# Optimization experiments

Hardware: AMD Instinct MI355X
Metric: run time of the kernel (lower is better)

Reference implementation:

```python
import jax, jax.numpy as jnp
import numpy as np

N_NODES = 50000
N_EDGES = 600000
IN_DIM = 128
H_DIM = 128
OUT_DIM = 128
N_REL = 8
N_BASES = 8
N_GRAPHS = 256


def _lin(key, i, o):
    return jax.random.normal(key, (i, o), dtype=jnp.float32) / np.sqrt(i)


def setup_inputs() -> dict:
    key = jax.random.key(0)
    ks = jax.random.split(key, 16)
    inp = {}
    inp["features"] = jax.random.normal(ks[0], (N_NODES, IN_DIM), dtype=jnp.float32)
    inp["src"] = jax.random.randint(ks[1], (N_EDGES,), 0, N_NODES, dtype=jnp.int32)
    inp["dst"] = jax.random.randint(ks[2], (N_EDGES,), 0, N_NODES, dtype=jnp.int32)
    inp["etype"] = jax.random.randint(ks[3], (N_EDGES,), 0, N_REL, dtype=jnp.int32)
    inp["node2graph"] = jnp.sort(jax.random.randint(ks[4], (N_NODES,), 0, N_GRAPHS, dtype=jnp.int32))
    # RelGraphConv basis-decomposed weights: bases [B,in,out], comp [R,B], bias [out]
    inp["bases1"] = jax.random.normal(ks[5], (N_BASES, IN_DIM, H_DIM), dtype=jnp.float32) / np.sqrt(IN_DIM)
    inp["comp1"] = jax.random.normal(ks[6], (N_REL, N_BASES), dtype=jnp.float32) / np.sqrt(N_BASES)
    inp["bias1"] = jnp.zeros((H_DIM,), dtype=jnp.float32)
    inp["bases2"] = jax.random.normal(ks[7], (N_BASES, H_DIM, H_DIM), dtype=jnp.float32) / np.sqrt(H_DIM)
    inp["comp2"] = jax.random.normal(ks[8], (N_REL, N_BASES), dtype=jnp.float32) / np.sqrt(N_BASES)
    inp["bias2"] = jnp.zeros((H_DIM,), dtype=jnp.float32)
    inp["bases3"] = jax.random.normal(ks[9], (N_BASES, H_DIM, OUT_DIM), dtype=jnp.float32) / np.sqrt(H_DIM)
    inp["comp3"] = jax.random.normal(ks[10], (N_REL, N_BASES), dtype=jnp.float32) / np.sqrt(N_BASES)
    inp["bias3"] = jnp.zeros((OUT_DIM,), dtype=jnp.float32)
    # attention gate + MLP head
    inp["gate_w"] = _lin(ks[11], OUT_DIM, 1)
    inp["gate_b"] = jnp.zeros((1,), dtype=jnp.float32)
    inp["fc1_w"] = _lin(ks[12], OUT_DIM, 100)
    inp["fc1_b"] = jnp.zeros((100,), dtype=jnp.float32)
    inp["fc2_w"] = _lin(ks[13], 100, 64)
    inp["fc2_b"] = jnp.zeros((64,), dtype=jnp.float32)
    inp["fc3_w"] = _lin(ks[14], 64, 1)
    inp["fc3_b"] = jnp.zeros((1,), dtype=jnp.float32)
    return inp


def _rgcn_layer(x, bases, comp, bias, src, dst, etype):
    # basis decomposition: W_r = sum_b comp[r,b] * bases[b]
    W = jnp.einsum('rb,bio->rio', comp, bases)            # [R, in, out]
    h_all = jnp.einsum('ni,rio->nro', x, W)               # [N, R, out]
    msg = h_all[src, etype]                               # gather per-edge: W_{etype} x_src, [E, out]
    agg = jax.ops.segment_sum(msg, dst, num_segments=x.shape[0])
    return agg + bias


def _segment_softmax(gate, seg, num_segments):
    # gate: [N, 1]; softmax per graph segment
    m = jax.ops.segment_max(gate, seg, num_segments=num_segments)
    e = jnp.exp(gate - m[seg])
    s = jax.ops.segment_sum(e, seg, num_segments=num_segments)
    return e / s[seg]


def reference(features, bases1, comp1, bias1, bases2, comp2, bias2,
              bases3, comp3, bias3, gate_w, gate_b,
              fc1_w, fc1_b, fc2_w, fc2_b, fc3_w, fc3_b,
              src, dst, etype, node2graph):
    h = _rgcn_layer(features, bases1, comp1, bias1, src, dst, etype)
    h = jax.nn.relu(h)  # dropout=0.0 -> identity
    h = _rgcn_layer(h, bases2, comp2, bias2, src, dst, etype)
    h = jax.nn.relu(h)
    h = _rgcn_layer(h, bases3, comp3, bias3, src, dst, etype)
    # GlobalAttentionPooling
    gate = h @ gate_w + gate_b                            # [N, 1]
    gate = _segment_softmax(gate, node2graph, N_GRAPHS)
    readout = jax.ops.segment_sum(h * gate, node2graph, num_segments=N_GRAPHS)  # [G, out]
    # MLP classifier + sigmoid
    z = jax.nn.relu(readout @ fc1_w + fc1_b)
    z = jax.nn.relu(z @ fc2_w + fc2_b)
    z = z @ fc3_w + fc3_b
    return jax.nn.sigmoid(z).squeeze(-1)                  # [G]
```

## Files before the change

### kernel.cpp

```cpp
#include <hip/hip_runtime.h>
#include <hip/hip_bf16.h>
#include <math.h>

#define N_NODES 50000
#define N_EDGES 600000
#define DIM 128
#define N_REL 8
#define N_GRAPHS 256
#define NBN 32
#define NBLK ((N_NODES + NBN - 1) / NBN)
#define KDIM (N_REL * DIM)
#define NKEY (N_NODES * N_REL)
#define SEG 1024
#define NSEG2 391

typedef __attribute__((ext_vector_type(8))) short short8;
typedef __attribute__((ext_vector_type(4))) float floatx4;
typedef __attribute__((ext_vector_type(4))) float f32x4;
typedef unsigned int uint;
typedef unsigned short ushort;

static __device__ __forceinline__ int lower_bound_i(const int* a, int n, int v) {
    int lo = 0, hi = n;
    while (lo < hi) { int mid = (lo + hi) >> 1; if (a[mid] < v) lo = mid + 1; else hi = mid; }
    return lo;
}

static __device__ __forceinline__ uint2 split2(float x, float y) {
    uint ux = __float_as_uint(x);
    uint hx = (ux + 0x7FFFu + ((ux >> 16) & 1u)) & 0xFFFF0000u;
    float rx = x - __uint_as_float(hx);
    uint urx = __float_as_uint(rx);
    uint lx = (urx + 0x7FFFu + ((urx >> 16) & 1u)) >> 16;
    uint uy = __float_as_uint(y);
    uint hy = (uy + 0x7FFFu + ((uy >> 16) & 1u)) & 0xFFFF0000u;
    float ry = y - __uint_as_float(hy);
    uint ury = __float_as_uint(ry);
    uint ly = (ury + 0x7FFFu + ((ury >> 16) & 1u)) >> 16;
    return make_uint2((hx >> 16) | (hy & 0xFFFF0000u), lx | (ly << 16));
}

__global__ void k_count(const int* __restrict__ dst, const int* __restrict__ etype,
                        int* __restrict__ counts, int e) {
    int i = blockIdx.x * blockDim.x + threadIdx.x;
    if (i < e) atomicAdd(&counts[dst[i] * 8 + etype[i]], 1);
}

__global__ __launch_bounds__(256) void k_scan_seg(const int* __restrict__ counts,
                                                  int* __restrict__ segscan,
                                                  int* __restrict__ segtot) {
    const int b = blockIdx.x, t = threadIdx.x;
    const int base = b * SEG + t * 4;
    const int4 v = *(const int4*)(counts + base);
    const int s0 = v.x, s1 = s0 + v.y, s2 = s1 + v.z, s3 = s2 + v.w;
    __shared__ int sl[256];
    sl[t] = s3;
    __syncthreads();
    for (int off = 1; off < 256; off <<= 1) {
        int add = (t >= off) ? sl[t - off] : 0;
        __syncthreads();
        sl[t] += add;
        __syncthreads();
    }
    const int tp = sl[t] - s3;
    int4 o;
    o.x = tp; o.y = tp + s0; o.z = tp + s1; o.w = tp + s2;
    *(int4*)(segscan + base) = o;
    if (t == 255) segtot[b] = sl[255];
}

__global__ __launch_bounds__(512) void k_scan_tot(const int* __restrict__ segtot,
                                                  int* __restrict__ segbase) {
    const int t = threadIdx.x;
    const int v = (t < NSEG2) ? segtot[t] : 0;
    __shared__ int sl[512];
    sl[t] = v;
    __syncthreads();
    for (int off = 1; off < 512; off <<= 1) {
        int u = (t >= off) ? sl[t - off] : 0;
        __syncthreads();
        sl[t] += u;
        __syncthreads();
    }
    if (t < NSEG2) segbase[t] = sl[t] - v;
    if (t == NSEG2) segbase[NSEG2] = sl[NSEG2 - 1];
}

__global__ void k_scan_fin(const int* __restrict__ segscan, const int* __restrict__ segbase,
                           int* __restrict__ offsets, int* __restrict__ cursor) {
    const int i = blockIdx.x * blockDim.x + threadIdx.x;
    if (i < NKEY) {
        const int val = segbase[i >> 10] + segscan[i];
        offsets[i] = val;
        cursor[i] = val;
    } else if (i == NKEY) {
        offsets[NKEY] = segbase[NSEG2];
    }
}

__global__ void k_fill(const int* __restrict__ src, const int* __restrict__ dst,
                       const int* __restrict__ etype, int* cursor,
                       int* __restrict__ edges, int e) {
    int i = blockIdx.x * blockDim.x + threadIdx.x;
    if (i < e) {
        const int et = etype[i];
        int pos = atomicAdd(&cursor[dst[i] * 8 + et], 1);
        edges[pos] = src[i] | (et << 16);
    }
}

__global__ void k_packW(const float* __restrict__ bases, const float* __restrict__ comp,
                        ushort* __restrict__ Whi, ushort* __restrict__ Wlo) {
    int id = blockIdx.x * blockDim.x + threadIdx.x;
    int nn = id & 127, k = id >> 7;
    int r = k >> 7, dk = k & 127;
    const float* cp = comp + r * 8;
    float v = 0.f;
#pragma unroll
    for (int b = 0; b < 8; b++) v = fmaf(cp[b], bases[((size_t)b * 128 + dk) * 128 + nn], v);
    uint u = __float_as_uint(v);
    uint hu = (u + 0x7FFFu + ((u >> 16) & 1u)) & 0xFFFF0000u;
    float rf = v - __uint_as_float(hu);
    uint ur = __float_as_uint(rf);
    uint lu = (ur + 0x7FFFu + ((ur >> 16) & 1u)) >> 16;
    int kt = k >> 5, kk = k & 31;
    int off = kt * 4096 + nn * 32 + kk;
    Whi[off] = (ushort)(hu >> 16);
    Wlo[off] = (ushort)lu;
}

template <bool RELU, bool GATE>
__global__ __launch_bounds__(512, 4) void k_layer(
    const float* __restrict__ xin, float* __restrict__ hout,
    const int* __restrict__ edges, const int* __restrict__ offsets,
    const ushort* __restrict__ Whi, const ushort* __restrict__ Wlo,
    const float* __restrict__ bias,
    const float* __restrict__ gw, const float* __restrict__ gb,
    float* __restrict__ gate) {
    __shared__ ushort sHi[16 * 1024];
    __shared__ ushort sLo[16 * 1024];
    __shared__ float sgatep[NBN][8];
    const int tid = threadIdx.x;
    const int lane = tid & 63;
    const int w = tid >> 6;
    const int q2 = lane >> 4, mm = lane & 15;
    const int xev = (mm ^ q2) * 8;
    const int xod = ((mm ^ q2) ^ 4) * 8;
    const int aq = q2 * 256;
    const int n0 = w * 16 + mm;
    const ushort* bph = Whi + n0 * 32 + q2 * 8;
    const ushort* bpl = Wlo + n0 * 32 + q2 * 8;
    floatx4 acc0 = {0.f, 0.f, 0.f, 0.f};
    floatx4 acc1 = {0.f, 0.f, 0.f, 0.f};

    const int hw = tid >> 5, l5 = tid & 31;
    const int d0 = l5 * 4;
    const int kt_off = l5 >> 3;
    const int q = (l5 >> 1) & 3;
    const int jb = (l5 & 1) * 4;

#pragma unroll
    for (int h = 0; h < 2; ++h) {
        {
            uint4 z = make_uint4(0u, 0u, 0u, 0u);
#pragma unroll
            for (int i = 0; i < 4; ++i) {
                ((uint4*)sHi)[tid + i * 512] = z;
                ((uint4*)sLo)[tid + i * 512] = z;
            }
        }
        __syncthreads();

        for (int v = 0; v < 2; ++v) {
            const int m = hw * 2 + v;
            const int n = blockIdx.x * NBN + m;
            int e0 = 0, e1 = 0;
            if (n < N_NODES) { e0 = offsets[n * 8 + h * 4]; e1 = offsets[n * 8 + h * 4 + 4]; }
            f32x4 tmp = (f32x4)0.f;
            int rcur = -1;

#define FLUSH_FRAG(RRR)                                                        \
            {                                                                  \
                const int ktp = (RRR) * 4 + kt_off;                            \
                const int chunk = q * 32 + ((m ^ q) ^ ((ktp & 1) << 2));       \
                const int uoff = ktp * 1024 + chunk * 8 + jb;                  \
                const uint2 p01 = split2(tmp.x, tmp.y);                        \
                const uint2 p23 = split2(tmp.z, tmp.w);                        \
                *(uint2*)(sHi + uoff) = make_uint2(p01.x, p23.x);              \
                *(uint2*)(sLo + uoff) = make_uint2(p01.y, p23.y);              \
            }

#define CONSUME_EDGE(PK, VV)                                                   \
            {                                                                  \
                const int r_ = ((PK) >> 16) & 3;                               \
                if (r_ != rcur) {                                              \
                    if (rcur >= 0) FLUSH_FRAG(rcur);                           \
                    rcur = r_;                                                 \
                    tmp = (VV);                                                \
                } else {                                                       \
                    tmp += (VV);                                               \
                }                                                              \
            }

            const int nb4 = (e1 - e0) >> 2;
            int pa0 = 0, pa1 = 0, pa2 = 0, pa3 = 0;
            int pb0 = 0, pb1 = 0, pb2 = 0, pb3 = 0;
            f32x4 va0, va1, va2, va3;
            if (0 < nb4) { const int ee = e0;     pa0 = edges[ee]; pa1 = edges[ee + 1]; pa2 = edges[ee + 2]; pa3 = edges[ee + 3]; }
            if (1 < nb4) { const int ee = e0 + 4; pb0 = edges[ee]; pb1 = edges[ee + 1]; pb2 = edges[ee + 2]; pb3 = edges[ee + 3]; }
            if (0 < nb4) {
                va0 = *(const f32x4*)(xin + (size_t)(pa0 & 0xFFFF) * DIM + d0);
                va1 = *(const f32x4*)(xin + (size_t)(pa1 & 0xFFFF) * DIM + d0);
                va2 = *(const f32x4*)(xin + (size_t)(pa2 & 0xFFFF) * DIM + d0);
                va3 = *(const f32x4*)(xin + (size_t)(pa3 & 0xFFFF) * DIM + d0);
            }
            for (int i = 0; i < nb4; ++i) {
                int pc0 = 0, pc1 = 0, pc2 = 0, pc3 = 0;
                if (i + 2 < nb4) {
                    const int ee = e0 + (i + 2) * 4;
                    pc0 = edges[ee]; pc1 = edges[ee + 1]; pc2 = edges[ee + 2]; pc3 = edges[ee + 3];
                }
                f32x4 vb0, vb1, vb2, vb3;
                if (i + 1 < nb4) {
                    vb0 = *(const f32x4*)(xin + (size_t)(pb0 & 0xFFFF) * DIM + d0);
                    vb1 = *(const f32x4*)(xin + (size_t)(pb1 & 0xFFFF) * DIM + d0);
                    vb2 = *(const f32x4*)(xin + (size_t)(pb2 & 0xFFFF) * DIM + d0);
                    vb3 = *(const f32x4*)(xin + (size_t)(pb3 & 0xFFFF) * DIM + d0);
                }
                CONSUME_EDGE(pa0, va0);
                CONSUME_EDGE(pa1, va1);
                CONSUME_EDGE(pa2, va2);
                CONSUME_EDGE(pa3, va3);
                pa0 = pb0; pa1 = pb1; pa2 = pb2; pa3 = pb3;
                pb0 = pc0; pb1 = pc1; pb2 = pc2; pb3 = pc3;
                va0 = vb0; va1 = vb1; va2 = vb2; va3 = vb3;
            }
            {
                const int et = e0 + nb4 * 4;
                const int rem = e1 - et;
                int pt0 = 0, pt1 = 0, pt2 = 0;
                if (rem > 0) pt0 = edges[et];
                if (rem > 1) pt1 = edges[et + 1];
                if (rem > 2) pt2 = edges[et + 2];
                f32x4 vt0, vt1, vt2;
                if (rem > 0) vt0 = *(const f32x4*)(xin + (size_t)(pt0 & 0xFFFF) * DIM + d0);
                if (rem > 1) vt1 = *(const f32x4*)(xin + (size_t)(pt1 & 0xFFFF) * DIM + d0);
                if (rem > 2) vt2 = *(const f32x4*)(xin + (size_t)(pt2 & 0xFFFF) * DIM + d0);
                if (rem > 0) CONSUME_EDGE(pt0, vt0);
                if (rem > 1) CONSUME_EDGE(pt1, vt1);
                if (rem > 2) CONSUME_EDGE(pt2, vt2);
            }
            if (rcur >= 0) FLUSH_FRAG(rcur);
#undef CONSUME_EDGE
#undef FLUSH_FRAG
        }
        __syncthreads();

        for (int kt = 0; kt < 16; kt += 2) {
            {
                const int ktg = h * 16 + kt;
                const ushort* ap = sHi + kt * 1024 + aq;
                const ushort* alp = sLo + kt * 1024 + aq;
                const short8 ah0 = *(const short8*)(ap + xev);
                const short8 ah1 = *(const short8*)(ap + 128 + xev);
                const short8 al0 = *(const short8*)(alp + xev);
                const short8 al1 = *(const short8*)(alp + 128 + xev);
                const short8 bh = *(const short8*)(bph + ktg * 4096);
                const short8 bl = *(const short8*)(bpl + ktg * 4096);
                acc0 = __builtin_amdgcn_mfma_f32_16x16x32_bf16(ah0, bh, acc0, 0, 0, 0);
                acc1 = __builtin_amdgcn_mfma_f32_16x16x32_bf16(ah1, bh, acc1, 0, 0, 0);
                acc0 = __builtin_amdgcn_mfma_f32_16x16x32_bf16(ah0, bl, acc0, 0, 0, 0);
                acc1 = __builtin_amdgcn_mfma_f32_16x16x32_bf16(ah1, bl, acc1, 0, 0, 0);
                acc0 = __builtin_amdgcn_mfma_f32_16x16x32_bf16(al0, bh, acc0, 0, 0, 0);
                acc1 = __builtin_amdgcn_mfma_f32_16x16x32_bf16(al1, bh, acc1, 0, 0, 0);
            }
            {
                const int kto = kt + 1;
                const int ktg = h * 16 + kto;
                const ushort* ap = sHi + kto * 1024 + aq;
                const ushort* alp = sLo + kto * 1024 + aq;
                const short8 ah0 = *(const short8*)(ap + xod);
                const short8 ah1 = *(const short8*)(ap + 128 + xod);
                const short8 al0 = *(const short8*)(alp + xod);
                const short8 al1 = *(const short8*)(alp + 128 + xod);
                const short8 bh = *(const short8*)(bph + ktg * 4096);
                const short8 bl = *(const short8*)(bpl + ktg * 4096);
                acc0 = __builtin_amdgcn_mfma_f32_16x16x32_bf16(ah0, bh, acc0, 0, 0, 0);
                acc1 = __builtin_amdgcn_mfma_f32_16x16x32_bf16(ah1, bh, acc1, 0, 0, 0);
                acc0 = __builtin_amdgcn_mfma_f32_16x16x32_bf16(ah0, bl, acc0, 0, 0, 0);
                acc1 = __builtin_amdgcn_mfma_f32_16x16x32_bf16(ah1, bl, acc1, 0, 0, 0);
                acc0 = __builtin_amdgcn_mfma_f32_16x16x32_bf16(al0, bh, acc0, 0, 0, 0);
                acc1 = __builtin_amdgcn_mfma_f32_16x16x32_bf16(al1, bh, acc1, 0, 0, 0);
            }
        }
        if (h == 0) __syncthreads();
    }

    const float b0 = bias[n0];
    float gp0[4], gp1[4];
#pragma unroll
    for (int r = 0; r < 4; r++) {
        const int row0 = q2 * 4 + r;
        const int nodeA = blockIdx.x * NBN + row0;
        const int nodeB = nodeA + 16;
        float v0 = acc0[r] + b0;
        float v1 = acc1[r] + b0;
        if (RELU) { v0 = fmaxf(v0, 0.f); v1 = fmaxf(v1, 0.f); }
        if (nodeA < N_NODES) hout[(size_t)nodeA * DIM + n0] = v0;
        if (nodeB < N_NODES) hout[(size_t)nodeB * DIM + n0] = v1;
        if (GATE) { gp0[r] = v0 * gw[n0]; gp1[r] = v1 * gw[n0]; }
    }
    if (GATE) {
#pragma unroll
        for (int r = 0; r < 4; r++) {
#pragma unroll
            for (int s = 1; s < 16; s <<= 1) {
                gp0[r] += __shfl_xor(gp0[r], s, 16);
                gp1[r] += __shfl_xor(gp1[r], s, 16);
            }
        }
        if (mm == 0) {
#pragma unroll
            for (int r = 0; r < 4; r++) {
                sgatep[q2 * 4 + r][w] = gp0[r];
                sgatep[16 + q2 * 4 + r][w] = gp1[r];
            }
        }
        __syncthreads();
        if (tid < NBN) {
            const int n = blockIdx.x * NBN + tid;
            if (n < N_NODES) {
                float s = 0.f;
#pragma unroll
                for (int w8 = 0; w8 < 8; w8++) s += sgatep[tid][w8];
                gate[n] = s + gb[0];
            }
        }
    }
}

__global__ __launch_bounds__(256) void k_pool(
    const float* __restrict__ h3, const float* __restrict__ gate, const int* __restrict__ n2g,
    const float* __restrict__ fc1w, const float* __restrict__ fc1b,
    const float* __restrict__ fc2w, const float* __restrict__ fc2b,
    const float* __restrict__ fc3w, const float* __restrict__ fc3b,
    float* __restrict__ out, int N) {
    const int g = blockIdx.x;
    const int tid = threadIdx.x;
    __shared__ float sred[256];
    __shared__ float sr[128];
    __shared__ float sz1[100];
    __shared__ float sz2[64];
    __shared__ float sm, ssum;

    const int s = lower_bound_i(n2g, N, g);
    const int e = lower_bound_i(n2g, N, g + 1);

    float m = -3.4e38f;
    for (int n = s + tid; n < e; n += 256) m = fmaxf(m, gate[n]);
    sred[tid] = m;
    __syncthreads();
    for (int off = 128; off > 0; off >>= 1) {
        if (tid < off) sred[tid] = fmaxf(sred[tid], sred[tid + off]);
        __syncthreads();
    }
    if (tid == 0) sm = sred[0];
    __syncthreads();
    const float mm = sm;

    float sum = 0.f;
    for (int n = s + tid; n < e; n += 256) sum += expf(gate[n] - mm);
    sred[tid] = sum;
    __syncthreads();
    for (int off = 128; off > 0; off >>= 1) {
        if (tid < off) sred[tid] += sred[tid + off];
        __syncthreads();
    }
    if (tid == 0) ssum = sred[0];
    __syncthreads();
    const float inv = (e > s) ? 1.0f / ssum : 0.f;

    const int col = tid & 127;
    const int half = tid >> 7;
    float acc = 0.f;
    int n = s + half;
    for (; n + 2 < e; n += 4) {
        const float w0 = expf(gate[n] - mm);
        const float w1 = expf(gate[n + 2] - mm);
        const float a0 = h3[(size_t)n * DIM + col];
        const float a1 = h3[(size_t)(n + 2) * DIM + col];
        acc = fmaf(w0, a0, acc);
        acc = fmaf(w1, a1, acc);
    }
    for (; n < e; n += 2) {
        const float wgt = expf(gate[n] - mm);
        acc = fmaf(wgt, h3[(size_t)n * DIM + col], acc);
    }
    sred[tid] = acc;
    __syncthreads();
    if (tid < 128) sr[tid] = (sred[tid] + sred[tid + 128]) * inv;
    __syncthreads();

    if (tid < 100) {
        float t = fc1b[tid];
        for (int i = 0; i < 128; i++) t = fmaf(sr[i], fc1w[i * 100 + tid], t);
        sz1[tid] = fmaxf(t, 0.f);
    }
    __syncthreads();
    if (tid < 64) {
        float t = fc2b[tid];
        for (int i = 0; i < 100; i++) t = fmaf(sz1[i], fc2w[i * 64 + tid], t);
        sz2[tid] = fmaxf(t, 0.f);
    }
    __syncthreads();
    if (tid < 64) {
        float p = sz2[tid] * fc3w[tid];
#pragma unroll
        for (int off = 32; off > 0; off >>= 1) p += __shfl_down(p, off, 64);
        if (tid == 0) {
            const float z = p + fc3b[0];
            out[g] = 1.0f / (1.0f + expf(-z));
        }
    }
}

extern "C" void kernel_launch(void* const* d_in, const int* in_sizes, int n_in,
                              void* d_out, int out_size, void* d_ws, size_t ws_size,
                              hipStream_t stream) {
    (void)in_sizes; (void)n_in; (void)out_size; (void)ws_size;
    const float* features = (const float*)d_in[0];
    const int*   src      = (const int*)d_in[1];
    const int*   dst      = (const int*)d_in[2];
    const int*   etype    = (const int*)d_in[3];
    const int*   n2g      = (const int*)d_in[4];
    const float* bases1   = (const float*)d_in[5];
    const float* comp1    = (const float*)d_in[6];
    const float* bias1    = (const float*)d_in[7];
    const float* bases2   = (const float*)d_in[8];
    const float* comp2    = (const float*)d_in[9];
    const float* bias2    = (const float*)d_in[10];
    const float* bases3   = (const float*)d_in[11];
    const float* comp3    = (const float*)d_in[12];
    const float* bias3    = (const float*)d_in[13];
    const float* gate_w   = (const float*)d_in[14];
    const float* gate_b   = (const float*)d_in[15];
    const float* fc1w     = (const float*)d_in[16];
    const float* fc1b     = (const float*)d_in[17];
    const float* fc2w     = (const float*)d_in[18];
    const float* fc2b     = (const float*)d_in[19];
    const float* fc3w     = (const float*)d_in[20];
    const float* fc3b     = (const float*)d_in[21];
    float* out = (float*)d_out;

    char* w = (char*)d_ws;
    auto alloc = [&](size_t bytes) -> char* {
        char* p = w;
        w += (bytes + 255) & ~(size_t)255;
        return p;
    };
    int*    offsets = (int*)alloc((NKEY + 1) * sizeof(int));
    int*    edges   = (int*)alloc(N_EDGES * sizeof(int));
    float*  hA      = (float*)alloc((size_t)N_NODES * DIM * sizeof(float));
    float*  hB      = (float*)alloc((size_t)N_NODES * DIM * sizeof(float));
    float*  gate    = (float*)alloc(N_NODES * sizeof(float));
    ushort* Whi1    = (ushort*)alloc((size_t)KDIM * DIM * sizeof(ushort));
    ushort* Wlo1    = (ushort*)alloc((size_t)KDIM * DIM * sizeof(ushort));
    ushort* Whi2    = (ushort*)alloc((size_t)KDIM * DIM * sizeof(ushort));
    ushort* Wlo2    = (ushort*)alloc((size_t)KDIM * DIM * sizeof(ushort));
    ushort* Whi3    = (ushort*)alloc((size_t)KDIM * DIM * sizeof(ushort));
    ushort* Wlo3    = (ushort*)alloc((size_t)KDIM * DIM * sizeof(ushort));
    int*    cursor  = (int*)hB;
    int*    segscan = (int*)((char*)hB + (2u << 20));
    int*    segtot  = (int*)((char*)hB + (4u << 20));
    int*    segbase = (int*)((char*)hB + (4u << 20) + 4096);

    k_packW<<<(KDIM * DIM) / 256, 256, 0, stream>>>(bases1, comp1, Whi1, Wlo1);
    k_packW<<<(KDIM * DIM) / 256, 256, 0, stream>>>(bases2, comp2, Whi2, Wlo2);
    k_packW<<<(KDIM * DIM) / 256, 256, 0, stream>>>(bases3, comp3, Whi3, Wlo3);

    hipMemsetAsync(cursor, 0, (size_t)NSEG2 * SEG * sizeof(int), stream);
    k_count<<<(N_EDGES + 255) / 256, 256, 0, stream>>>(dst, etype, cursor, N_EDGES);
    k_scan_seg<<<NSEG2, 256, 0, stream>>>(cursor, segscan, segtot);
    k_scan_tot<<<1, 512, 0, stream>>>(segtot, segbase);
    k_scan_fin<<<(NKEY + 256) / 256, 256, 0, stream>>>(segscan, segbase, offsets, cursor);
    k_fill<<<(N_EDGES + 255) / 256, 256, 0, stream>>>(src, dst, etype, cursor, edges, N_EDGES);

    k_layer<true, false><<<NBLK, 512, 0, stream>>>(features, hA, edges, offsets, Whi1, Wlo1, bias1, gate_w, gate_b, gate);
    k_layer<true, false><<<NBLK, 512, 0, stream>>>(hA, hB, edges, offsets, Whi2, Wlo2, bias2, gate_w, gate_b, gate);
    k_layer<false, true><<<NBLK, 512, 0, stream>>>(hB, hA, edges, offsets, Whi3, Wlo3, bias3, gate_w, gate_b, gate);

    k_pool<<<N_GRAPHS, 256, 0, stream>>>(hA, gate, n2g, fc1w, fc1b, fc2w, fc2b, fc3w, fc3b, out, N_NODES);
}
```

Baseline: 532.4 us.

## Process relations in pairs with smaller LDS tiles and fuse weight packing

The layer kernel now walks relations two at a time over four rounds, accumulating each relation's neighbour sum in registers and writing only two fragments to LDS, instead of zeroing and filling a 16-tile buffer per half. This halves shared memory per block and raises the launch-bound occupancy hint so more waves can hide gather latency, at the cost of an extra barrier per round and a simpler edge loop without software prefetch. The three weight-packing launches are merged into one kernel, the pooling loop is unrolled further, and the edges buffer gets padding.

```diff
diff --git a/kernel.cpp b/kernel.cpp
--- a/kernel.cpp
+++ b/kernel.cpp
@@ -109,9 +109,18 @@
     }
 }
 
-__global__ void k_packW(const float* __restrict__ bases, const float* __restrict__ comp,
-                        ushort* __restrict__ Whi, ushort* __restrict__ Wlo) {
-    int id = blockIdx.x * blockDim.x + threadIdx.x;
+__global__ void k_packW3(const float* __restrict__ b1, const float* __restrict__ c1,
+                         ushort* __restrict__ Whi1, ushort* __restrict__ Wlo1,
+                         const float* __restrict__ b2, const float* __restrict__ c2,
+                         ushort* __restrict__ Whi2, ushort* __restrict__ Wlo2,
+                         const float* __restrict__ b3, const float* __restrict__ c3,
+                         ushort* __restrict__ Whi3, ushort* __restrict__ Wlo3) {
+    const int lay = blockIdx.x >> 9;
+    const int id = (blockIdx.x & 511) * blockDim.x + threadIdx.x;
+    const float* bases = (lay == 0) ? b1 : (lay == 1) ? b2 : b3;
+    const float* comp  = (lay == 0) ? c1 : (lay == 1) ? c2 : c3;
+    ushort* Whi = (lay == 0) ? Whi1 : (lay == 1) ? Whi2 : Whi3;
+    ushort* Wlo = (lay == 0) ? Wlo1 : (lay == 1) ? Wlo2 : Wlo3;
     int nn = id & 127, k = id >> 7;
     int r = k >> 7, dk = k & 127;
     const float* cp = comp + r * 8;
@@ -130,15 +139,15 @@
 }
 
 template <bool RELU, bool GATE>
-__global__ __launch_bounds__(512, 4) void k_layer(
+__global__ __launch_bounds__(512, 8) void k_layer(
     const float* __restrict__ xin, float* __restrict__ hout,
     const int* __restrict__ edges, const int* __restrict__ offsets,
     const ushort* __restrict__ Whi, const ushort* __restrict__ Wlo,
     const float* __restrict__ bias,
     const float* __restrict__ gw, const float* __restrict__ gb,
     float* __restrict__ gate) {
-    __shared__ ushort sHi[16 * 1024];
-    __shared__ ushort sLo[16 * 1024];
+    __shared__ ushort sHi[8 * 1024];
+    __shared__ ushort sLo[8 * 1024];
     __shared__ float sgatep[NBN][8];
     const int tid = threadIdx.x;
     const int lane = tid & 63;
@@ -159,106 +168,52 @@
     const int q = (l5 >> 1) & 3;
     const int jb = (l5 & 1) * 4;
 
-#pragma unroll
-    for (int h = 0; h < 2; ++h) {
-        {
-            uint4 z = make_uint4(0u, 0u, 0u, 0u);
-#pragma unroll
-            for (int i = 0; i < 4; ++i) {
-                ((uint4*)sHi)[tid + i * 512] = z;
-                ((uint4*)sLo)[tid + i * 512] = z;
-            }
-        }
-        __syncthreads();
-
+    for (int ro = 0; ro < 4; ++ro) {
         for (int v = 0; v < 2; ++v) {
             const int m = hw * 2 + v;
             const int n = blockIdx.x * NBN + m;
-            int e0 = 0, e1 = 0;
-            if (n < N_NODES) { e0 = offsets[n * 8 + h * 4]; e1 = offsets[n * 8 + h * 4 + 4]; }
-            f32x4 tmp = (f32x4)0.f;
-            int rcur = -1;
-
-#define FLUSH_FRAG(RRR)                                                        \
-            {                                                                  \
-                const int ktp = (RRR) * 4 + kt_off;                            \
-                const int chunk = q * 32 + ((m ^ q) ^ ((ktp & 1) << 2));       \
-                const int uoff = ktp * 1024 + chunk * 8 + jb;                  \
-                const uint2 p01 = split2(tmp.x, tmp.y);                        \
-                const uint2 p23 = split2(tmp.z, tmp.w);                        \
-                *(uint2*)(sHi + uoff) = make_uint2(p01.x, p23.x);              \
-                *(uint2*)(sLo + uoff) = make_uint2(p01.y, p23.y);              \
-            }
-
-#define CONSUME_EDGE(PK, VV)                                                   \
-            {                                                                  \
-                const int r_ = ((PK) >> 16) & 3;                               \
-                if (r_ != rcur) {                                              \
-                    if (rcur >= 0) FLUSH_FRAG(rcur);                           \
-                    rcur = r_;                                                 \
-                    tmp = (VV);                                                \
-                } else {                                                       \
-                    tmp += (VV);                                               \
-                }                                                              \
-            }
-
-            const int nb4 = (e1 - e0) >> 2;
-            int pa0 = 0, pa1 = 0, pa2 = 0, pa3 = 0;
-            int pb0 = 0, pb1 = 0, pb2 = 0, pb3 = 0;
-            f32x4 va0, va1, va2, va3;
-            if (0 < nb4) { const int ee = e0;     pa0 = edges[ee]; pa1 = edges[ee + 1]; pa2 = edges[ee + 2]; pa3 = edges[ee + 3]; }
-            if (1 < nb4) { const int ee = e0 + 4; pb0 = edges[ee]; pb1 = edges[ee + 1]; pb2 = edges[ee + 2]; pb3 = edges[ee + 3]; }
-            if (0 < nb4) {
-                va0 = *(const f32x4*)(xin + (size_t)(pa0 & 0xFFFF) * DIM + d0);
-                va1 = *(const f32x4*)(xin + (size_t)(pa1 & 0xFFFF) * DIM + d0);
-                va2 = *(const f32x4*)(xin + (size_t)(pa2 & 0xFFFF) * DIM + d0);
-                va3 = *(const f32x4*)(xin + (size_t)(pa3 & 0xFFFF) * DIM + d0);
-            }
-            for (int i = 0; i < nb4; ++i) {
-                int pc0 = 0, pc1 = 0, pc2 = 0, pc3 = 0;
-                if (i + 2 < nb4) {
-                    const int ee = e0 + (i + 2) * 4;
-                    pc0 = edges[ee]; pc1 = edges[ee + 1]; pc2 = edges[ee + 2]; pc3 = edges[ee + 3];
-                }
-                f32x4 vb0, vb1, vb2, vb3;
-                if (i + 1 < nb4) {
-                    vb0 = *(const f32x4*)(xin + (size_t)(pb0 & 0xFFFF) * DIM + d0);
-                    vb1 = *(const f32x4*)(xin + (size_t)(pb1 & 0xFFFF) * DIM + d0);
-                    vb2 = *(const f32x4*)(xin + (size_t)(pb2 & 0xFFFF) * DIM + d0);
-                    vb3 = *(const f32x4*)(xin + (size_t)(pb3 & 0xFFFF) * DIM + d0);
-                }
-                CONSUME_EDGE(pa0, va0);
-                CONSUME_EDGE(pa1, va1);
-                CONSUME_EDGE(pa2, va2);
-                CONSUME_EDGE(pa3, va3);
-                pa0 = pb0; pa1 = pb1; pa2 = pb2; pa3 = pb3;
-                pb0 = pc0; pb1 = pc1; pb2 = pc2; pb3 = pc3;
-                va0 = vb0; va1 = vb1; va2 = vb2; va3 = vb3;
+            int e = 0, e1 = 0;
+            if (n < N_NODES) { e = offsets[n * 8 + ro * 2]; e1 = offsets[n * 8 + ro * 2 + 2]; }
+            f32x4 a0 = (f32x4)0.f, a1 = (f32x4)0.f;
+            while (e < e1) {
+                const int c = e1 - e;
+                const int p0 = edges[e];
+                const int p1 = (c > 1) ? edges[e + 1] : 0;
+                const int p2 = (c > 2) ? edges[e + 2] : 0;
+                const int p3 = (c > 3) ? edges[e + 3] : 0;
+                f32x4 v0, v1, v2, v3;
+                v0 = *(const f32x4*)(xin + (size_t)(p0 & 0xFFFF) * DIM + d0);
+                if (c > 1) v1 = *(const f32x4*)(xin + (size_t)(p1 & 0xFFFF) * DIM + d0);
+                if (c > 2) v2 = *(const f32x4*)(xin + (size_t)(p2 & 0xFFFF) * DIM + d0);
+                if (c > 3) v3 = *(const f32x4*)(xin + (size_t)(p3 & 0xFFFF) * DIM + d0);
+                if (p0 & 0x10000) a1 += v0; else a0 += v0;
+                if (c > 1) { if (p1 & 0x10000) a1 += v1; else a0 += v1; }
+                if (c > 2) { if (p2 & 0x10000) a1 += v2; else a0 += v2; }
+                if (c > 3) { if (p3 & 0x10000) a1 += v3; else a0 += v3; }
+                e += 4;
             }
             {
-                const int et = e0 + nb4 * 4;
-                const int rem = e1 - et;
-                int pt0 = 0, pt1 = 0, pt2 = 0;
-                if (rem > 0) pt0 = edges[et];
-                if (rem > 1) pt1 = edges[et + 1];
-                if (rem > 2) pt2 = edges[et + 2];
-                f32x4 vt0, vt1, vt2;
-                if (rem > 0) vt0 = *(const f32x4*)(xin + (size_t)(pt0 & 0xFFFF) * DIM + d0);
-                if (rem > 1) vt1 = *(const f32x4*)(xin + (size_t)(pt1 & 0xFFFF) * DIM + d0);
-                if (rem > 2) vt2 = *(const f32x4*)(xin + (size_t)(pt2 & 0xFFFF) * DIM + d0);
-                if (rem > 0) CONSUME_EDGE(pt0, vt0);
-                if (rem > 1) CONSUME_EDGE(pt1, vt1);
-                if (rem > 2) CONSUME_EDGE(pt2, vt2);
-            }
-            if (rcur >= 0) FLUSH_FRAG(rcur);
-#undef CONSUME_EDGE
-#undef FLUSH_FRAG
-        }
-        __syncthreads();
-
-        for (int kt = 0; kt < 16; kt += 2) {
+                const int ktp0 = kt_off;
+                const int ch0 = q * 32 + ((m ^ q) ^ ((ktp0 & 1) << 2));
+                const int u0 = ktp0 * 1024 + ch0 * 8 + jb;
+                const uint2 h01 = split2(a0.x, a0.y);
+                const uint2 h23 = split2(a0.z, a0.w);
+                *(uint2*)(sHi + u0) = make_uint2(h01.x, h23.x);
+                *(uint2*)(sLo + u0) = make_uint2(h01.y, h23.y);
+                const int ktp1 = 4 + kt_off;
+                const int ch1 = q * 32 + ((m ^ q) ^ ((ktp1 & 1) << 2));
+                const int u1 = ktp1 * 1024 + ch1 * 8 + jb;
+                const uint2 g01 = split2(a1.x, a1.y);
+                const uint2 g23 = split2(a1.z, a1.w);
+                *(uint2*)(sHi + u1) = make_uint2(g01.x, g23.x);
+                *(uint2*)(sLo + u1) = make_uint2(g01.y, g23.y);
+            }
+        }
+        __syncthreads();
+
+        for (int kt = 0; kt < 8; kt += 2) {
             {
-                const int ktg = h * 16 + kt;
+                const int ktg = ro * 8 + kt;
                 const ushort* ap = sHi + kt * 1024 + aq;
                 const ushort* alp = sLo + kt * 1024 + aq;
                 const short8 ah0 = *(const short8*)(ap + xev);
@@ -276,7 +231,7 @@
             }
             {
                 const int kto = kt + 1;
-                const int ktg = h * 16 + kto;
+                const int ktg = ro * 8 + kto;
                 const ushort* ap = sHi + kto * 1024 + aq;
                 const ushort* alp = sLo + kto * 1024 + aq;
                 const short8 ah0 = *(const short8*)(ap + xod);
@@ -293,7 +248,7 @@
                 acc1 = __builtin_amdgcn_mfma_f32_16x16x32_bf16(al1, bh, acc1, 0, 0, 0);
             }
         }
-        if (h == 0) __syncthreads();
+        if (ro < 3) __syncthreads();
     }
 
     const float b0 = bias[n0];
@@ -319,6 +274,7 @@
                 gp1[r] += __shfl_xor(gp1[r], s, 16);
             }
         }
+        __syncthreads();
         if (mm == 0) {
 #pragma unroll
             for (int r = 0; r < 4; r++) {
@@ -384,13 +340,19 @@
     const int half = tid >> 7;
     float acc = 0.f;
     int n = s + half;
-    for (; n + 2 < e; n += 4) {
+    for (; n + 6 < e; n += 8) {
         const float w0 = expf(gate[n] - mm);
         const float w1 = expf(gate[n + 2] - mm);
+        const float w2 = expf(gate[n + 4] - mm);
+        const float w3 = expf(gate[n + 6] - mm);
         const float a0 = h3[(size_t)n * DIM + col];
         const float a1 = h3[(size_t)(n + 2) * DIM + col];
+        const float a2 = h3[(size_t)(n + 4) * DIM + col];
+        const float a3 = h3[(size_t)(n + 6) * DIM + col];
         acc = fmaf(w0, a0, acc);
         acc = fmaf(w1, a1, acc);
+        acc = fmaf(w2, a2, acc);
+        acc = fmaf(w3, a3, acc);
     }
     for (; n < e; n += 2) {
         const float wgt = expf(gate[n] - mm);
@@ -459,7 +421,7 @@
         return p;
     };
     int*    offsets = (int*)alloc((NKEY + 1) * sizeof(int));
-    int*    edges   = (int*)alloc(N_EDGES * sizeof(int));
+    int*    edges   = (int*)alloc((N_EDGES + 16) * sizeof(int));
     float*  hA      = (float*)alloc((size_t)N_NODES * DIM * sizeof(float));
     float*  hB      = (float*)alloc((size_t)N_NODES * DIM * sizeof(float));
     float*  gate    = (float*)alloc(N_NODES * sizeof(float));
@@ -474,9 +436,9 @@
     int*    segtot  = (int*)((char*)hB + (4u << 20));
     int*    segbase = (int*)((char*)hB + (4u << 20) + 4096);
 
-    k_packW<<<(KDIM * DIM) / 256, 256, 0, stream>>>(bases1, comp1, Whi1, Wlo1);
-    k_packW<<<(KDIM * DIM) / 256, 256, 0, stream>>>(bases2, comp2, Whi2, Wlo2);
-    k_packW<<<(KDIM * DIM) / 256, 256, 0, stream>>>(bases3, comp3, Whi3, Wlo3);
+    k_packW3<<<1536, 256, 0, stream>>>(bases1, comp1, Whi1, Wlo1,
+                                       bases2, comp2, Whi2, Wlo2,
+                                       bases3, comp3, Whi3, Wlo3);
 
     hipMemsetAsync(cursor, 0, (size_t)NSEG2 * SEG * sizeof(int), stream);
     k_count<<<(N_EDGES + 255) / 256, 256, 0, stream>>>(dst, etype, cursor, N_EDGES);
```

Result: faster. 460.4 us (-13.5%).
